# Kernel optimization log

Hardware: AMD Instinct MI355X
Metric: run time of the kernel (lower is better)

The kernel has to match this reference:

```python
import jax, jax.numpy as jnp
import numpy as np

N, D = 65536, 256


def _unit(x):
    # contrastive embeddings are L2-normalized; also keeps exp(dot) finite
    return x / jnp.linalg.norm(x, axis=-1, keepdims=True)


def setup_inputs() -> dict:
    key = jax.random.key(0)
    k1, k2 = jax.random.split(key)
    z_a = _unit(jax.random.normal(k1, (N, D), dtype=jnp.float32))
    z_b = _unit(jax.random.normal(k2, (N, D), dtype=jnp.float32))
    return {"z_a": z_a, "z_b": z_b}


def reference(z_a, z_b):
    # d_i = dot(z_a[i], z_b[i])  (the only quantity the original ever computes)
    n = z_a.shape[0]
    d = jnp.sum(z_a * z_b, axis=-1)  # [n]
    # Original loop structure:
    #   alignment      = sum_i (-d_i)
    #   negative_sum_i = (# of j in range(n-1), j != i) * d_i
    #                  = (n-2) * d_i for i < n-1, (n-1) * d_i for i == n-1
    #   uniformity_i   = exp(d_i)
    counts = jnp.full((n,), n - 2, dtype=d.dtype).at[n - 1].set(n - 1)
    return jnp.sum((counts - 1.0) * d + jnp.exp(d))
```

## Files before the change

kernel.cpp:

```cpp
#include <hip/hip_runtime.h>
#include <math.h>


#define D_DIM 256
#define MAIN_BLOCKS 2048
#define WAVES_PER_BLOCK 4

__global__ __launch_bounds__(256)
void dot_loss_partial(const float* __restrict__ za,
                      const float* __restrict__ zb,
                      float* __restrict__ partial,
                      int n) {
    const int lane = threadIdx.x & 63;
    const int wave = threadIdx.x >> 6;
    const int rowStart = blockIdx.x * WAVES_PER_BLOCK + wave;
    const int rowStride = gridDim.x * WAVES_PER_BLOCK;

    float acc = 0.0f;

    for (int row = rowStart; row < n; row += rowStride) {
        const float4* a4 = (const float4*)(za + (size_t)row * D_DIM);
        const float4* b4 = (const float4*)(zb + (size_t)row * D_DIM);
        float4 av = a4[lane];
        float4 bv = b4[lane];
        float d = av.x * bv.x;
        d = fmaf(av.y, bv.y, d);
        d = fmaf(av.z, bv.z, d);
        d = fmaf(av.w, bv.w, d);
        #pragma unroll
        for (int off = 32; off > 0; off >>= 1)
            d += __shfl_down(d, off);
        if (lane == 0) {
            float coeff = (row == n - 1) ? (float)(n - 2) : (float)(n - 3);
            acc = fmaf(coeff, d, acc) + expf(d) - 0.0f;
        }
    }

    __shared__ float smem[WAVES_PER_BLOCK];
    if (lane == 0) smem[wave] = acc;
    __syncthreads();
    if (threadIdx.x == 0) {
        float s = 0.0f;
        #pragma unroll
        for (int w = 0; w < WAVES_PER_BLOCK; ++w) s += smem[w];
        partial[blockIdx.x] = s;
    }
}

__global__ __launch_bounds__(256)
void reduce_partials(const float* __restrict__ partial,
                     float* __restrict__ out,
                     int m) {
    const int lane = threadIdx.x & 63;
    const int wave = threadIdx.x >> 6;
    double s = 0.0;
    for (int i = threadIdx.x; i < m; i += 256)
        s += (double)partial[i];
    #pragma unroll
    for (int off = 32; off > 0; off >>= 1)
        s += __shfl_down(s, off);
    __shared__ double smem[4];
    if (lane == 0) smem[wave] = s;
    __syncthreads();
    if (threadIdx.x == 0)
        out[0] = (float)(smem[0] + smem[1] + smem[2] + smem[3]);
}

extern "C" void kernel_launch(void* const* d_in, const int* in_sizes, int n_in,
                              void* d_out, int out_size, void* d_ws, size_t ws_size,
                              hipStream_t stream) {
    const float* za = (const float*)d_in[0];
    const float* zb = (const float*)d_in[1];
    float* out = (float*)d_out;
    float* partial = (float*)d_ws;
    const int n = in_sizes[0] / D_DIM;

    dot_loss_partial<<<MAIN_BLOCKS, 256, 0, stream>>>(za, zb, partial, n);
    reduce_partials<<<1, 256, 0, stream>>>(partial, out, MAIN_BLOCKS);
}
```

Baseline: 147.1 us.

## Batch four rows per wave and replace second reduction kernel with atomicAdd

Each wave now loads four rows of both inputs up front and interleaves their shuffle reductions, so more memory requests are in flight per wave. The grid-stride loop is replaced by a fixed grid sized for N, and the separate partial-reduction kernel is replaced by a memset plus one float atomicAdd per block. This drops one kernel launch and the workspace round-trip. In exchange, the grid now hard-codes the row count, there are no bounds checks, and float atomics make the summation order nondeterministic with slightly different rounding.

```diff
diff --git a/kernel.cpp b/kernel.cpp
--- a/kernel.cpp
+++ b/kernel.cpp
@@ -3,67 +3,60 @@
 
 
 #define D_DIM 256
-#define MAIN_BLOCKS 2048
-#define WAVES_PER_BLOCK 4
+#define ROWS 4
+#define BLOCKS 4096
 
 __global__ __launch_bounds__(256)
-void dot_loss_partial(const float* __restrict__ za,
-                      const float* __restrict__ zb,
-                      float* __restrict__ partial,
-                      int n) {
+void dot_loss(const float* __restrict__ za,
+              const float* __restrict__ zb,
+              float* __restrict__ out,
+              int n) {
     const int lane = threadIdx.x & 63;
     const int wave = threadIdx.x >> 6;
-    const int rowStart = blockIdx.x * WAVES_PER_BLOCK + wave;
-    const int rowStride = gridDim.x * WAVES_PER_BLOCK;
+    const int waveId = blockIdx.x * 4 + wave;
+    const int row0 = waveId * ROWS;
+
+    const float4* a4 = (const float4*)za + (size_t)row0 * 64 + lane;
+    const float4* b4 = (const float4*)zb + (size_t)row0 * 64 + lane;
+
+    float4 av[ROWS], bv[ROWS];
+    #pragma unroll
+    for (int r = 0; r < ROWS; ++r) av[r] = a4[(size_t)r * 64];
+    #pragma unroll
+    for (int r = 0; r < ROWS; ++r) bv[r] = b4[(size_t)r * 64];
+
+    float d[ROWS];
+    #pragma unroll
+    for (int r = 0; r < ROWS; ++r) {
+        float t = av[r].x * bv[r].x;
+        t = fmaf(av[r].y, bv[r].y, t);
+        t = fmaf(av[r].z, bv[r].z, t);
+        t = fmaf(av[r].w, bv[r].w, t);
+        d[r] = t;
+    }
+
+    #pragma unroll
+    for (int off = 32; off > 0; off >>= 1) {
+        #pragma unroll
+        for (int r = 0; r < ROWS; ++r)
+            d[r] += __shfl_down(d[r], off);
+    }
 
     float acc = 0.0f;
-
-    for (int row = rowStart; row < n; row += rowStride) {
-        const float4* a4 = (const float4*)(za + (size_t)row * D_DIM);
-        const float4* b4 = (const float4*)(zb + (size_t)row * D_DIM);
-        float4 av = a4[lane];
-        float4 bv = b4[lane];
-        float d = av.x * bv.x;
-        d = fmaf(av.y, bv.y, d);
-        d = fmaf(av.z, bv.z, d);
-        d = fmaf(av.w, bv.w, d);
+    if (lane == 0) {
         #pragma unroll
-        for (int off = 32; off > 0; off >>= 1)
-            d += __shfl_down(d, off);
-        if (lane == 0) {
+        for (int r = 0; r < ROWS; ++r) {
+            int row = row0 + r;
             float coeff = (row == n - 1) ? (float)(n - 2) : (float)(n - 3);
-            acc = fmaf(coeff, d, acc) + expf(d) - 0.0f;
+            acc += coeff * d[r] + expf(d[r]);
         }
     }
 
-    __shared__ float smem[WAVES_PER_BLOCK];
+    __shared__ float smem[4];
     if (lane == 0) smem[wave] = acc;
     __syncthreads();
-    if (threadIdx.x == 0) {
-        float s = 0.0f;
-        #pragma unroll
-        for (int w = 0; w < WAVES_PER_BLOCK; ++w) s += smem[w];
-        partial[blockIdx.x] = s;
-    }
-}
-
-__global__ __launch_bounds__(256)
-void reduce_partials(const float* __restrict__ partial,
-                     float* __restrict__ out,
-                     int m) {
-    const int lane = threadIdx.x & 63;
-    const int wave = threadIdx.x >> 6;
-    double s = 0.0;
-    for (int i = threadIdx.x; i < m; i += 256)
-        s += (double)partial[i];
-    #pragma unroll
-    for (int off = 32; off > 0; off >>= 1)
-        s += __shfl_down(s, off);
-    __shared__ double smem[4];
-    if (lane == 0) smem[wave] = s;
-    __syncthreads();
     if (threadIdx.x == 0)
-        out[0] = (float)(smem[0] + smem[1] + smem[2] + smem[3]);
+        atomicAdd(out, smem[0] + smem[1] + smem[2] + smem[3]);
 }
 
 extern "C" void kernel_launch(void* const* d_in, const int* in_sizes, int n_in,
@@ -72,9 +65,8 @@
     const float* za = (const float*)d_in[0];
     const float* zb = (const float*)d_in[1];
     float* out = (float*)d_out;
-    float* partial = (float*)d_ws;
     const int n = in_sizes[0] / D_DIM;
 
-    dot_loss_partial<<<MAIN_BLOCKS, 256, 0, stream>>>(za, zb, partial, n);
-    reduce_partials<<<1, 256, 0, stream>>>(partial, out, MAIN_BLOCKS);
+    hipMemsetAsync(out, 0, sizeof(float), stream);
+    dot_loss<<<BLOCKS, 256, 0, stream>>>(za, zb, out, n);
 }
```

Result: slower. 165.2 us (+12.3%).

## Batch 32 rows per wave and reduce dot products through LDS transpose

Applied to the files above, without the earlier changes.

Each wave now owns a contiguous block of 32 rows and issues all of their loads up front (unrolled by 8), instead of one row per grid-stride iteration. Per-lane partial products go to padded shared memory, and the wave reads them back transposed, so each lane sums half a row and one shuffle finishes it. This replaces the six-step shuffle reduction per row and raises memory-level parallelism. In exchange it uses about 33KB of LDS per block, assumes n is divisible by 128, and the grid size now depends on n. Only a wave-local wait orders the LDS writes and reads, with no barrier.

```diff
diff --git a/kernel.cpp b/kernel.cpp
--- a/kernel.cpp
+++ b/kernel.cpp
@@ -3,47 +3,64 @@
 
 
 #define D_DIM 256
-#define MAIN_BLOCKS 2048
+#define ROWS_PER_WAVE 32
 #define WAVES_PER_BLOCK 4
 
-__global__ __launch_bounds__(256)
-void dot_loss_partial(const float* __restrict__ za,
-                      const float* __restrict__ zb,
+__global__ __launch_bounds__(256, 2)
+void dot_loss_partial(const float4* __restrict__ za4,
+                      const float4* __restrict__ zb4,
                       float* __restrict__ partial,
                       int n) {
     const int lane = threadIdx.x & 63;
     const int wave = threadIdx.x >> 6;
-    const int rowStart = blockIdx.x * WAVES_PER_BLOCK + wave;
-    const int rowStride = gridDim.x * WAVES_PER_BLOCK;
+    const int waveId = blockIdx.x * WAVES_PER_BLOCK + wave;
+    const int row0 = waveId * ROWS_PER_WAVE;
+
+    __shared__ float part[WAVES_PER_BLOCK][ROWS_PER_WAVE][65];
+
+    const float4* a = za4 + (size_t)row0 * 64 + lane;
+    const float4* b = zb4 + (size_t)row0 * 64 + lane;
+
+    #pragma unroll 8
+    for (int r = 0; r < ROWS_PER_WAVE; ++r) {
+        float4 av = a[(size_t)r * 64];
+        float4 bv = b[(size_t)r * 64];
+        float t = av.x * bv.x;
+        t = fmaf(av.y, bv.y, t);
+        t = fmaf(av.z, bv.z, t);
+        t = fmaf(av.w, bv.w, t);
+        part[wave][r][lane] = t;
+    }
+    __builtin_amdgcn_s_waitcnt(0);
+
+    const int rowIdx = lane & 31;
+    const int colBase = (lane >> 5) * 32;
+    float s = 0.0f;
+    #pragma unroll
+    for (int c = 0; c < 32; ++c)
+        s += part[wave][rowIdx][colBase + c];
+
+    float d = s + __shfl_down(s, 32);
 
     float acc = 0.0f;
+    if (lane < 32) {
+        int row = row0 + rowIdx;
+        float coeff = (row == n - 1) ? (float)(n - 2) : (float)(n - 3);
+        acc = coeff * d + expf(d);
+    }
 
-    for (int row = rowStart; row < n; row += rowStride) {
-        const float4* a4 = (const float4*)(za + (size_t)row * D_DIM);
-        const float4* b4 = (const float4*)(zb + (size_t)row * D_DIM);
-        float4 av = a4[lane];
-        float4 bv = b4[lane];
-        float d = av.x * bv.x;
-        d = fmaf(av.y, bv.y, d);
-        d = fmaf(av.z, bv.z, d);
-        d = fmaf(av.w, bv.w, d);
-        #pragma unroll
-        for (int off = 32; off > 0; off >>= 1)
-            d += __shfl_down(d, off);
-        if (lane == 0) {
-            float coeff = (row == n - 1) ? (float)(n - 2) : (float)(n - 3);
-            acc = fmaf(coeff, d, acc) + expf(d) - 0.0f;
-        }
-    }
+    #pragma unroll
+    for (int off = 16; off > 0; off >>= 1)
+        acc += __shfl_down(acc, off);
 
     __shared__ float smem[WAVES_PER_BLOCK];
     if (lane == 0) smem[wave] = acc;
     __syncthreads();
     if (threadIdx.x == 0) {
-        float s = 0.0f;
+        float s2 = 0.0f;
         #pragma unroll
-        for (int w = 0; w < WAVES_PER_BLOCK; ++w) s += smem[w];
-        partial[blockIdx.x] = s;
+        for (int w = 0; w < WAVES_PER_BLOCK; ++w) s2 += smem[w];
+        partial[blockIdx.x] = s2;
     }
 }
 
@@ -69,12 +86,13 @@
 extern "C" void kernel_launch(void* const* d_in, const int* in_sizes, int n_in,
                               void* d_out, int out_size, void* d_ws, size_t ws_size,
                               hipStream_t stream) {
-    const float* za = (const float*)d_in[0];
-    const float* zb = (const float*)d_in[1];
+    const float4* za4 = (const float4*)d_in[0];
+    const float4* zb4 = (const float4*)d_in[1];
     float* out = (float*)d_out;
     float* partial = (float*)d_ws;
     const int n = in_sizes[0] / D_DIM;
+    const int blocks = n / (ROWS_PER_WAVE * WAVES_PER_BLOCK);
 
-    dot_loss_partial<<<MAIN_BLOCKS, 256, 0, stream>>>(za, zb, partial, n);
-    reduce_partials<<<1, 256, 0, stream>>>(partial, out, MAIN_BLOCKS);
+    dot_loss_partial<<<blocks, 256, 0, stream>>>(za4, zb4, partial, n);
+    reduce_partials<<<1, 256, 0, stream>>>(partial, out, blocks);
 }
```

Result: faster. 143.6 us (-2.3%).
